# Performance work log

Measured on AMD Instinct MI355X. Metric: run time of the kernel, lower is better.

Reference implementation:

```python
import jax, jax.numpy as jnp
import numpy as np
from jax import lax
from jax.scipy.special import logsumexp

B, S, H, L = 64, 512, 1024, 9

def setup_inputs() -> dict:
    key = jax.random.key(0)
    ks = jax.random.split(key, 7)
    return {
        'sequence_output': jax.random.normal(ks[0], (B, S, H), dtype=jnp.float32),
        'tags': jax.random.randint(ks[1], (B, S), 0, L, dtype=jnp.int32),
        'mask': jnp.ones((B, S), dtype=bool),
        'W': jax.random.normal(ks[2], (L, H), dtype=jnp.float32) * 0.02,
        'b': jax.random.normal(ks[3], (L,), dtype=jnp.float32) * 0.02,
        'start_transitions': jax.random.normal(ks[4], (L,), dtype=jnp.float32) * 0.1,
        'end_transitions': jax.random.normal(ks[5], (L,), dtype=jnp.float32) * 0.1,
        'transitions': jax.random.normal(ks[6], (L,), dtype=jnp.float32).repeat(1) if False else jax.random.normal(ks[6], (L, L), dtype=jnp.float32) * 0.1,
    }

def _crf_nll(emissions, tags, mask, start_transitions, end_transitions, transitions):
    # emissions: [B,S,L], tags: [B,S] int, mask: [B,S] bool (mask[:,0] all True)
    Bn, Sn, Ln = emissions.shape
    maskf = mask.astype(emissions.dtype)
    bidx = jnp.arange(Bn)
    # ---- numerator: score of the gold tag sequence ----
    score = start_transitions[tags[:, 0]] + emissions[bidx, 0, tags[:, 0]]
    trans_sc = transitions[tags[:, :-1], tags[:, 1:]]                      # [B,S-1]
    emit_sc = jnp.take_along_axis(emissions, tags[..., None].astype(jnp.int32), axis=2)[..., 0]  # [B,S]
    score = score + jnp.sum((trans_sc + emit_sc[:, 1:]) * maskf[:, 1:], axis=1)
    seq_ends = jnp.sum(mask.astype(jnp.int32), axis=1) - 1                 # [B]
    last_tags = tags[bidx, seq_ends]
    score = score + end_transitions[last_tags]
    # ---- denominator: log partition via forward algorithm (scan over time) ----
    em_t = jnp.swapaxes(emissions, 0, 1)   # [S,B,L]
    mk_t = jnp.swapaxes(mask, 0, 1)        # [S,B]
    alpha0 = start_transitions + em_t[0]   # [B,L]
    def step(alpha, xs):
        em, m = xs
        nxt = logsumexp(alpha[:, :, None] + transitions[None] + em[:, None, :], axis=1)
        alpha = jnp.where(m[:, None], nxt, alpha)
        return alpha, None
    alpha, _ = lax.scan(step, alpha0, (em_t[1:], mk_t[1:]))
    logZ = logsumexp(alpha + end_transitions, axis=1)  # [B]
    llh = jnp.sum(score - logZ)  # reduction='sum'
    return -llh

def reference(sequence_output, tags, mask, W, b, start_transitions, end_transitions, transitions):
    # dropout is identity in eval/reference mode
    emissions = jnp.einsum('bsh,lh->bsl', sequence_output, W) + b
    return _crf_nll(emissions, tags, mask, start_transitions, end_transitions, transitions)
```

## Files before the change

kernel.cpp:

```cpp
#include <hip/hip_runtime.h>
#include <math.h>

#define Bn 64
#define Sn 512
#define Hn 1024
#define Ln 9
#define NC 32
#define KC 16


typedef __bf16 bf16x8 __attribute__((ext_vector_type(8)));
typedef unsigned short ushort8 __attribute__((ext_vector_type(8)));
typedef float f32x4 __attribute__((ext_vector_type(4)));

static __device__ __forceinline__ unsigned short f2bf(float x) {
  union { float f; unsigned u; } v; v.f = x;
  unsigned r = v.u + 0x7FFFu + ((v.u >> 16) & 1u);
  return (unsigned short)(r >> 16);
}

static __device__ __forceinline__ bf16x8 pack8(float4 a, float4 b) {
  ushort8 u;
  u[0] = f2bf(a.x); u[1] = f2bf(a.y); u[2] = f2bf(a.z); u[3] = f2bf(a.w);
  u[4] = f2bf(b.x); u[5] = f2bf(b.y); u[6] = f2bf(b.z); u[7] = f2bf(b.w);
  return __builtin_bit_cast(bf16x8, u);
}

__global__ __launch_bounds__(256, 2) void crf_emis(
    const float* __restrict__ seq, const float* __restrict__ W,
    const float* __restrict__ bias, float* __restrict__ emG) {
  const int tid  = threadIdx.x;
  const int lane = tid & 63;
  const int wv   = tid >> 6;
  const int tile = blockIdx.x * 4 + wv;
  const int col  = lane & 15;
  const int kg   = lane >> 4;
  const int wrow = (col < Ln) ? col : 0;

  bf16x8 wf[32];
#pragma unroll
  for (int ks = 0; ks < 32; ++ks) {
    const float* wp = W + wrow * Hn + ks * 32 + kg * 8;
    wf[ks] = pack8(*(const float4*)wp, *(const float4*)(wp + 4));
  }

  const int arow = lane & 15;
  const float* ap = seq + ((size_t)tile * 16 + arow) * Hn + kg * 8;

  f32x4 acc = {0.f, 0.f, 0.f, 0.f};
  float4 abuf[4][2];
#pragma unroll
  for (int p = 0; p < 3; ++p) {
    abuf[p][0] = *(const float4*)(ap + p * 32);
    abuf[p][1] = *(const float4*)(ap + p * 32 + 4);
  }
#pragma unroll
  for (int ks = 0; ks < 32; ++ks) {
    if (ks + 3 < 32) {
      abuf[(ks + 3) & 3][0] = *(const float4*)(ap + (ks + 3) * 32);
      abuf[(ks + 3) & 3][1] = *(const float4*)(ap + (ks + 3) * 32 + 4);
    }
    bf16x8 af = pack8(abuf[ks & 3][0], abuf[ks & 3][1]);
    acc = __builtin_amdgcn_mfma_f32_16x16x32_bf16(af, wf[ks], acc, 0, 0, 0);
  }

  if (col < Ln) {
    const float bv = bias[col];
    float* ep = emG + ((size_t)tile * 16 + kg * 4) * Ln + col;
#pragma unroll
    for (int r = 0; r < 4; ++r) ep[r * Ln] = acc[r] + bv;
  }
}

__global__ __launch_bounds__(128) void crf_chunk(
    const float* __restrict__ emG, const float* __restrict__ trans,
    const float* __restrict__ startT, float* __restrict__ Mall,
    float* __restrict__ alphaBuf) {
  const int bc = blockIdx.x;
  const int b = bc >> 5, c = bc & (NC - 1);
  const int tid = threadIdx.x;

  __shared__ float em_s[KC][Ln];
  __shared__ float Mlds[2][Ln][12];

  for (int i = tid; i < KC * Ln; i += 128)
    ((float*)em_s)[i] = emG[(size_t)bc * KC * Ln + i];
  __syncthreads();

  if (c == 0) {
    if (tid < 64) {
      const int lane = tid;
      const int j = (lane < Ln) ? lane : 0;
      float Tcol[Ln];
#pragma unroll
      for (int i = 0; i < Ln; ++i) Tcol[i] = trans[i * Ln + j];
      float alpha[Ln];
#pragma unroll
      for (int i = 0; i < Ln; ++i) alpha[i] = startT[i] + em_s[0][i];

      for (int t = 1; t < KC; ++t) {
        float m = alpha[0];
#pragma unroll
        for (int i = 1; i < Ln; ++i) m = fmaxf(m, alpha[i]);
        float s = 0.f;
#pragma unroll
        for (int i = 0; i < Ln; ++i) s += __expf(alpha[i] - m + Tcol[i]);
        float nxt = m + __logf(s) + em_s[t][j];
#pragma unroll
        for (int i = 0; i < Ln; ++i) alpha[i] = __shfl(nxt, i);
      }
      if (lane < Ln) alphaBuf[b * 16 + lane] = alpha[lane];
    }
  } else {
    const bool act = (tid < 81);
    const int i = tid / 9, j = tid - i * 9;
    float Treg[Ln];
    float val = 0.f;
    if (act) {
#pragma unroll
      for (int k = 0; k < Ln; ++k) Treg[k] = trans[k * Ln + j];
      val = trans[i * Ln + j] + em_s[0][j];
      Mlds[0][i][j] = val;
    }
    __syncthreads();

    int cur = 0;
    for (int t = 1; t < KC; ++t) {
      if (act) {
        float Mr[Ln];
#pragma unroll
        for (int k = 0; k < Ln; ++k) Mr[k] = Mlds[cur][i][k];
        float e = em_s[t][j];
        float m = Mr[0];
#pragma unroll
        for (int k = 1; k < Ln; ++k) m = fmaxf(m, Mr[k]);
        float s = 0.f;
#pragma unroll
        for (int k = 0; k < Ln; ++k) s += __expf(Mr[k] - m + Treg[k]);
        val = m + __logf(s) + e;
        Mlds[cur ^ 1][i][j] = val;
      }
      __syncthreads();
      cur ^= 1;
    }
    if (act) Mall[(size_t)bc * 81 + tid] = val;
  }
}

__global__ __launch_bounds__(64) void crf_combine(
    const float* __restrict__ Mall, const float* __restrict__ alphaBuf,
    const float* __restrict__ emG, const int* __restrict__ tags,
    const float* __restrict__ trans, const float* __restrict__ startT,
    const float* __restrict__ endT, float* __restrict__ out) {
  const int b = blockIdx.x;
  const int lane = threadIdx.x;

  float g = 0.f;
#pragma unroll
  for (int k = 0; k < 8; ++k) {
    const int t = lane + (k << 6);
    const int cur = tags[b * Sn + t];
    float add = emG[((size_t)b * Sn + t) * Ln + cur];
    if (t == 0) add += startT[cur];
    else add += trans[tags[b * Sn + t - 1] * Ln + cur];
    if (t == Sn - 1) add += endT[cur];
    g += add;
  }
#pragma unroll
  for (int off = 32; off > 0; off >>= 1) g += __shfl_xor(g, off);

  const int j = (lane < Ln) ? lane : 0;
  const float* Mb = Mall + (size_t)b * NC * 81;

  float alpha[Ln];
#pragma unroll
  for (int i = 0; i < Ln; ++i) alpha[i] = alphaBuf[b * 16 + i];

  float col[Ln];
#pragma unroll
  for (int i = 0; i < Ln; ++i) col[i] = Mb[81 + i * 9 + j];

  for (int cc = 1; cc < NC; ++cc) {
    float ncol[Ln];
    if (cc + 1 < NC) {
#pragma unroll
      for (int i = 0; i < Ln; ++i) ncol[i] = Mb[(cc + 1) * 81 + i * 9 + j];
    }
    float m = alpha[0];
#pragma unroll
    for (int i = 1; i < Ln; ++i) m = fmaxf(m, alpha[i]);
    float s = 0.f;
#pragma unroll
    for (int i = 0; i < Ln; ++i) s += __expf(alpha[i] - m + col[i]);
    float nxt = m + __logf(s);
#pragma unroll
    for (int i = 0; i < Ln; ++i) alpha[i] = __shfl(nxt, i);
#pragma unroll
    for (int i = 0; i < Ln; ++i) col[i] = ncol[i];
  }

  float mf = alpha[0] + endT[0];
#pragma unroll
  for (int i = 1; i < Ln; ++i) mf = fmaxf(mf, alpha[i] + endT[i]);
  float z = 0.f;
#pragma unroll
  for (int i = 0; i < Ln; ++i) z += __expf(alpha[i] + endT[i] - mf);
  float logZ = mf + __logf(z);

  if (lane == 0) atomicAdd(out, logZ - g);
}

extern "C" void kernel_launch(void* const* d_in, const int* in_sizes, int n_in,
                              void* d_out, int out_size, void* d_ws, size_t ws_size,
                              hipStream_t stream) {
  const float* seq    = (const float*)d_in[0];
  const int*   tags   = (const int*)d_in[1];
  const float* W      = (const float*)d_in[3];
  const float* bias   = (const float*)d_in[4];
  const float* startT = (const float*)d_in[5];
  const float* endT   = (const float*)d_in[6];
  const float* trans  = (const float*)d_in[7];

  float* em       = (float*)d_ws;
  float* Mall     = em + (size_t)Bn * Sn * Ln;
  float* alphaBuf = Mall + (size_t)Bn * NC * 81;

  crf_emis<<<512, 256, 0, stream>>>(seq, W, bias, em);
  crf_chunk<<<Bn * NC, 128, 0, stream>>>(em, trans, startT, Mall, alphaBuf);
  crf_combine<<<Bn, 64, 0, stream>>>(Mall, alphaBuf, em, tags, trans, startT,
                                     endT, (float*)d_out);
}
```

Before: 239.6 us.

## Split emission GEMM K dimension across waves with direct-to-LDS loads

Each block now handles a single 16-row tile, and its four waves each take a quarter of the hidden dimension. The A tile is copied straight into shared memory with global_load_lds, and partial MFMA accumulators are summed through LDS. The grid grows from 512 to 2048 blocks, which exposes more memory-level parallelism for streaming the 128MB input. The cost is an extra LDS reduction and barrier, and W is reloaded per block, though only a quarter of it per wave.

Result: faster. 230.7 us (-3.7%).

```diff
diff --git a/kernel.cpp b/kernel.cpp
--- a/kernel.cpp
+++ b/kernel.cpp
@@ -29,46 +29,70 @@
 __global__ __launch_bounds__(256, 2) void crf_emis(
     const float* __restrict__ seq, const float* __restrict__ W,
     const float* __restrict__ bias, float* __restrict__ emG) {
+  __shared__ float alds[4][8][2][64][4];
+  __shared__ float comb[4][64][4];
   const int tid  = threadIdx.x;
   const int lane = tid & 63;
   const int wv   = tid >> 6;
-  const int tile = blockIdx.x * 4 + wv;
+  const int tile = blockIdx.x;
   const int col  = lane & 15;
   const int kg   = lane >> 4;
-  const int wrow = (col < Ln) ? col : 0;
-
-  bf16x8 wf[32];
-#pragma unroll
-  for (int ks = 0; ks < 32; ++ks) {
-    const float* wp = W + wrow * Hn + ks * 32 + kg * 8;
-    wf[ks] = pack8(*(const float4*)wp, *(const float4*)(wp + 4));
-  }
-
-  const int arow = lane & 15;
-  const float* ap = seq + ((size_t)tile * 16 + arow) * Hn + kg * 8;
+  const int wcol = (col < Ln) ? col : 0;
+
+  const float* tb = seq + (size_t)tile * 16 * Hn;
+
+#pragma unroll
+  for (int k8 = 0; k8 < 8; ++k8) {
+    const int ks = wv * 8 + k8;
+#pragma unroll
+    for (int h = 0; h < 2; ++h) {
+      const float* src = tb + (size_t)col * Hn + ks * 32 + kg * 8 + h * 4;
+      __builtin_amdgcn_global_load_lds(
+          (const __attribute__((address_space(1))) void*)src,
+          (__attribute__((address_space(3))) void*)&alds[wv][k8][h][0][0],
+          16, 0, 0);
+    }
+  }
+
+  bf16x8 wf[8];
+#pragma unroll
+  for (int k8 = 0; k8 < 8; ++k8) {
+    const int ks = wv * 8 + k8;
+    const float* wp = W + (size_t)wcol * Hn + ks * 32 + kg * 8;
+    wf[k8] = pack8(*(const float4*)wp, *(const float4*)(wp + 4));
+  }
+
+  asm volatile("s_waitcnt vmcnt(0)" ::: "memory");
+  __builtin_amdgcn_sched_barrier(0);
 
   f32x4 acc = {0.f, 0.f, 0.f, 0.f};
-  float4 abuf[4][2];
-#pragma unroll
-  for (int p = 0; p < 3; ++p) {
-    abuf[p][0] = *(const float4*)(ap + p * 32);
-    abuf[p][1] = *(const float4*)(ap + p * 32 + 4);
-  }
-#pragma unroll
-  for (int ks = 0; ks < 32; ++ks) {
-    if (ks + 3 < 32) {
-      abuf[(ks + 3) & 3][0] = *(const float4*)(ap + (ks + 3) * 32);
-      abuf[(ks + 3) & 3][1] = *(const float4*)(ap + (ks + 3) * 32 + 4);
-    }
-    bf16x8 af = pack8(abuf[ks & 3][0], abuf[ks & 3][1]);
-    acc = __builtin_amdgcn_mfma_f32_16x16x32_bf16(af, wf[ks], acc, 0, 0, 0);
-  }
-
-  if (col < Ln) {
-    const float bv = bias[col];
-    float* ep = emG + ((size_t)tile * 16 + kg * 4) * Ln + col;
-#pragma unroll
-    for (int r = 0; r < 4; ++r) ep[r * Ln] = acc[r] + bv;
+#pragma unroll
+  for (int k8 = 0; k8 < 8; ++k8) {
+    float4 a0 = *(const float4*)&alds[wv][k8][0][lane][0];
+    float4 a1 = *(const float4*)&alds[wv][k8][1][lane][0];
+    acc = __builtin_amdgcn_mfma_f32_16x16x32_bf16(pack8(a0, a1), wf[k8],
+                                                  acc, 0, 0, 0);
+  }
+
+  *(float4*)&comb[wv][lane][0] = make_float4(acc[0], acc[1], acc[2], acc[3]);
+  __syncthreads();
+  if (wv == 0) {
+    float4 s0 = *(const float4*)&comb[0][lane][0];
+    float4 s1 = *(const float4*)&comb[1][lane][0];
+    float4 s2 = *(const float4*)&comb[2][lane][0];
+    float4 s3 = *(const float4*)&comb[3][lane][0];
+    float r0 = s0.x + s1.x + s2.x + s3.x;
+    float r1 = s0.y + s1.y + s2.y + s3.y;
+    float r2 = s0.z + s1.z + s2.z + s3.z;
+    float r3 = s0.w + s1.w + s2.w + s3.w;
+    if (col < Ln) {
+      const float bv = bias[col];
+      float* ep = emG + ((size_t)tile * 16 + kg * 4) * Ln + col;
+      ep[0 * Ln] = r0 + bv;
+      ep[1 * Ln] = r1 + bv;
+      ep[2 * Ln] = r2 + bv;
+      ep[3 * Ln] = r3 + bv;
+    }
   }
 }
 
@@ -225,7 +249,7 @@
   float* Mall     = em + (size_t)Bn * Sn * Ln;
   float* alphaBuf = Mall + (size_t)Bn * NC * 81;
 
-  crf_emis<<<512, 256, 0, stream>>>(seq, W, bias, em);
+  crf_emis<<<Bn * NC, 256, 0, stream>>>(seq, W, bias, em);
   crf_chunk<<<Bn * NC, 128, 0, stream>>>(em, trans, startT, Mall, alphaBuf);
   crf_combine<<<Bn, 64, 0, stream>>>(Mall, alphaBuf, em, tags, trans, startT,
                                      endT, (float*)d_out);
```
